# Kernel tuning notes

Measured on AMD Instinct MI355X. Metric: run time of the kernel, lower is better.

The kernel has to match this reference:

```python
import jax, jax.numpy as jnp
import numpy as np

BATCH, SEQ, NUM_SUB, CB_SIZE, SUB_DIM = 8, 2048, 16, 1024, 64
EMB_DIM = NUM_SUB * SUB_DIM  # 1024


def setup_inputs() -> dict:
    key = jax.random.key(0)
    k1, k2 = jax.random.split(key)
    embeddings = jax.random.normal(k1, (BATCH, SEQ, EMB_DIM), dtype=jnp.float32)
    # stacked PQ codebooks: [num_subspaces, codebook_size, subspace_dim]
    codebooks = jax.random.normal(k2, (NUM_SUB, CB_SIZE, SUB_DIM), dtype=jnp.float32)
    return {"embeddings": embeddings, "codebooks": codebooks}


def reference(embeddings, codebooks):
    B, S, D = embeddings.shape
    M, K, d = codebooks.shape
    # [N, M, d] tokens split into subspaces
    x = embeddings.reshape(-1, M, d)
    x2 = jnp.sum(x * x, axis=-1, keepdims=True)            # [N, M, 1]
    c2 = jnp.sum(codebooks * codebooks, axis=-1)           # [M, K]
    xc = jnp.einsum('nmd,mkd->nmk', x, codebooks)          # [N, M, K]
    dist2 = x2 - 2.0 * xc + c2[None, :, :]
    indices = jnp.argmin(dist2, axis=-1)                   # [N, M] (argmin of sqdist == argmin of cdist)
    # gather nearest codeword per subspace: [N, M, d]
    quantized = jnp.take_along_axis(
        codebooks[None, :, :, :],                          # [1, M, K, d]
        indices[:, :, None, None],                         # [N, M, 1, 1]
        axis=2,
    )[:, :, 0, :]
    quantized = quantized.reshape(B, S, D)
    indices = indices.reshape(B, S, M).astype(jnp.int64)
    return quantized, indices
```

## Files before the change

### kernel.cpp

```cpp
#include <hip/hip_runtime.h>
#include <hip/hip_bf16.h>

#pragma clang fp contract(off)

#define NSUB 16
#define CBK  1024
#define SDIM 64
#define EMB  1024
#define NTOK 16384
#define TOKB 128
#define MARGIN 5e-3f

typedef __attribute__((ext_vector_type(8))) short bf16x8;
typedef __attribute__((ext_vector_type(4))) float f32x4;

__device__ __forceinline__ float fmul(float a, float b) { return __fmul_rn(a, b); }
__device__ __forceinline__ float fadd(float a, float b) { return __fadd_rn(a, b); }
__device__ __forceinline__ float fsub(float a, float b) { return __fsub_rn(a, b); }

__device__ __forceinline__ float np_sq64(const float* v) {
    float r[8];
    #pragma unroll
    for (int j = 0; j < 8; ++j) r[j] = fmul(v[j], v[j]);
    #pragma unroll
    for (int b = 1; b < 8; ++b) {
        #pragma unroll
        for (int j = 0; j < 8; ++j)
            r[j] = fadd(r[j], fmul(v[b * 8 + j], v[b * 8 + j]));
    }
    return fadd(fadd(fadd(r[0], r[1]), fadd(r[2], r[3])),
                fadd(fadd(r[4], r[5]), fadd(r[6], r[7])));
}

__device__ __forceinline__ void split_bf16(float v, short& hi, short& lo) {
    __hip_bfloat16 h = __float2bfloat16(v);
    float hf = __bfloat162float(h);
    __hip_bfloat16 e = __float2bfloat16(__fsub_rn(v, hf));
    hi = *(short*)&h;
    lo = *(short*)&e;
}

typedef const __attribute__((address_space(1))) unsigned int gu32;
typedef __attribute__((address_space(3))) unsigned int lu32;
__device__ __forceinline__ void stage16(const void* g, void* l) {
    __builtin_amdgcn_global_load_lds((gu32*)g, (lu32*)l, 16, 0, 0);
}

__global__ __launch_bounds__(256)
void prep_kernel(const float* __restrict__ cb,
                 unsigned short* __restrict__ bpack,
                 float* __restrict__ c2g)
{
    const int bx = blockIdx.x;
    const int m  = blockIdx.y;
    const int t  = threadIdx.x;
    const int w  = t >> 6, l = t & 63;
    const int tc = bx * 2 + (w & 1);
    const int c  = w >> 1;
    const int cw = tc * 16 + (l & 15);
    const int dq = (l >> 4) * 8;

    {
        const float* src = cb + ((size_t)m * CBK + cw) * SDIM + c * 32 + dq;
        bf16x8 hv, lv;
        #pragma unroll
        for (int j = 0; j < 8; ++j) {
            short h, e; split_bf16(-2.0f * src[j], h, e);
            hv[j] = h; lv[j] = e;
        }
        size_t base = (((size_t)(m * 64 + tc) * 2 + c) * 2) * 512 + (size_t)l * 8;
        *(bf16x8*)(bpack + base)       = hv;
        *(bf16x8*)(bpack + base + 512) = lv;
    }
    if (t < 32) {
        const int row = bx * 32 + t;
        c2g[m * CBK + row] = np_sq64(cb + ((size_t)m * CBK + row) * SDIM);
    }
}

__global__ __launch_bounds__(256)
void idx_transpose_kernel(const float* __restrict__ iws,
                          float* __restrict__ iout)
{
    const int tok = blockIdx.x * 256 + threadIdx.x;
    float v[NSUB];
    #pragma unroll
    for (int m = 0; m < NSUB; ++m)
        v[m] = iws[(size_t)m * NTOK + tok];
    float* dst = iout + (size_t)tok * NSUB;
    #pragma unroll
    for (int c = 0; c < 4; ++c)
        *(f32x4*)(dst + c * 4) = *(f32x4*)(v + c * 4);
}

__global__ __launch_bounds__(256, 4)
void pq_mfma_kernel(const float* __restrict__ emb,
                    const float* __restrict__ cb,
                    const unsigned short* __restrict__ bpack,
                    const float* __restrict__ c2g,
                    float* __restrict__ qout,
                    float* __restrict__ iws)
{
    __shared__ __align__(16) unsigned short bs[2][4 * 2048];
    __shared__ float C2s[CBK];
    __shared__ int   bestk_s[TOKB];
    __shared__ int   flag_s[TOKB];
    __shared__ int   cnt_s;

    const int rank = blockIdx.x;
    const int m    = rank & 15;
    const int tok0 = (rank >> 4) * TOKB;

    const int t = threadIdx.x, w = t >> 6, l = t & 63;
    const int ln15 = l & 15, q = l >> 4;

    if (t == 0) cnt_s = 0;
    *(f32x4*)(C2s + t * 4) = *(const f32x4*)(c2g + m * CBK + t * 4);

    const unsigned short* gB = bpack + (size_t)m * 64 * 2048;

    {
        const unsigned short* src = gB + t * 8;
        #pragma unroll
        for (int j = 0; j < 4; ++j)
            stage16(src + j * 2048, &bs[0][j * 2048 + t * 8]);
    }

    bf16x8 xh[2][2], xl[2][2];
    #pragma unroll
    for (int r = 0; r < 2; ++r) {
        const int tok = tok0 + w * 32 + r * 16 + ln15;
        #pragma unroll
        for (int c = 0; c < 2; ++c) {
            const float* src = emb + (size_t)tok * EMB + m * SDIM + c * 32 + q * 8;
            float4 v0 = *(const float4*)(src);
            float4 v1 = *(const float4*)(src + 4);
            float vv[8] = {v0.x,v0.y,v0.z,v0.w,v1.x,v1.y,v1.z,v1.w};
            #pragma unroll
            for (int j = 0; j < 8; ++j) {
                short h, e; split_bf16(vv[j], h, e);
                xh[r][c][j] = h; xl[r][c][j] = e;
            }
        }
    }

    float v1t[2][4], v2t[2][4]; int k1t[2][4];
    #pragma unroll
    for (int r = 0; r < 2; ++r)
        #pragma unroll
        for (int g = 0; g < 4; ++g) { v1t[r][g] = 3.4e38f; v2t[r][g] = 3.4e38f; k1t[r][g] = 0; }

    __syncthreads();

#define COMPUTE_TILE(B0, B1, B2, B3, TC)                                        \
    {                                                                           \
        const int kk = (TC) * 16 + ln15;                                        \
        const float c2v = C2s[kk];                                              \
        _Pragma("unroll")                                                       \
        for (int r = 0; r < 2; ++r) {                                           \
            f32x4 acc = {c2v, c2v, c2v, c2v};                                   \
            acc = __builtin_amdgcn_mfma_f32_16x16x32_bf16(xh[r][0], B0, acc, 0, 0, 0); \
            acc = __builtin_amdgcn_mfma_f32_16x16x32_bf16(xh[r][1], B2, acc, 0, 0, 0); \
            acc = __builtin_amdgcn_mfma_f32_16x16x32_bf16(xl[r][0], B0, acc, 0, 0, 0); \
            acc = __builtin_amdgcn_mfma_f32_16x16x32_bf16(xl[r][1], B2, acc, 0, 0, 0); \
            acc = __builtin_amdgcn_mfma_f32_16x16x32_bf16(xh[r][0], B1, acc, 0, 0, 0); \
            acc = __builtin_amdgcn_mfma_f32_16x16x32_bf16(xh[r][1], B3, acc, 0, 0, 0); \
            _Pragma("unroll")                                                   \
            for (int g = 0; g < 4; ++g) {                                       \
                float s = acc[g];                                               \
                v2t[r][g] = fminf(v2t[r][g], fmaxf(s, v1t[r][g]));              \
                bool lt = s < v1t[r][g];                                        \
                v1t[r][g] = lt ? s : v1t[r][g];                                 \
                k1t[r][g] = lt ? kk : k1t[r][g];                                \
            }                                                                   \
        }                                                                       \
    }

    for (int ph = 0; ph < 16; ++ph) {
        const int buf = ph & 1;
        if (ph < 15) {
            const unsigned short* src = gB + (size_t)(ph + 1) * 8192 + t * 8;
            #pragma unroll
            for (int j = 0; j < 4; ++j)
                stage16(src + j * 2048, &bs[buf ^ 1][j * 2048 + t * 8]);
        }
        #pragma unroll
        for (int j = 0; j < 4; ++j) {
            const int tc = ph * 4 + j;
            const unsigned short* bp = &bs[buf][j * 2048 + l * 8];
            bf16x8 B0 = *(const bf16x8*)(bp);
            bf16x8 B1 = *(const bf16x8*)(bp + 512);
            bf16x8 B2 = *(const bf16x8*)(bp + 1024);
            bf16x8 B3 = *(const bf16x8*)(bp + 1536);
            COMPUTE_TILE(B0, B1, B2, B3, tc)
        }
        __syncthreads();
    }
#undef COMPUTE_TILE

    #pragma unroll
    for (int r = 0; r < 2; ++r) {
        #pragma unroll
        for (int g = 0; g < 4; ++g) {
            float v1 = v1t[r][g], v2 = v2t[r][g]; int k1 = k1t[r][g];
            #pragma unroll
            for (int mask = 1; mask < 16; mask <<= 1) {
                float ov1 = __shfl_xor(v1, mask);
                float ov2 = __shfl_xor(v2, mask);
                int   ok1 = __shfl_xor(k1, mask);
                if (ov1 < v1 || (ov1 == v1 && ok1 < k1)) {
                    v2 = fminf(v1, ov2);
                    v1 = ov1; k1 = ok1;
                } else {
                    v2 = fminf(v2, ov1);
                }
            }
            if (ln15 == 0) {
                const int token = w * 32 + r * 16 + q * 4 + g;
                if (v2 - v1 <= MARGIN) {
                    int slot = atomicAdd(&cnt_s, 1);
                    flag_s[slot] = token;
                } else {
                    bestk_s[token] = k1;
                    iws[(size_t)m * NTOK + tok0 + token] = (float)k1;
                }
            }
        }
    }
    __syncthreads();

    const int nflag = cnt_s;
    for (int g0 = w * 16; g0 < nflag; g0 += 64) {
        const int slotL = g0 + ln15;
        const int tokL  = flag_s[slotL < nflag ? slotL : g0];
        bf16x8 fxh[2], fxl[2];
        #pragma unroll
        for (int c = 0; c < 2; ++c) {
            const float* src = emb + (size_t)(tok0 + tokL) * EMB + m * SDIM + c * 32 + q * 8;
            float4 v0 = *(const float4*)(src);
            float4 v1 = *(const float4*)(src + 4);
            float vv[8] = {v0.x,v0.y,v0.z,v0.w,v1.x,v1.y,v1.z,v1.w};
            #pragma unroll
            for (int j = 0; j < 8; ++j) {
                short h, e; split_bf16(vv[j], h, e);
                fxh[c][j] = h; fxl[c][j] = e;
            }
        }

        unsigned long long cmask[4] = {0ull, 0ull, 0ull, 0ull};
        float v1r[4] = {3.4e38f, 3.4e38f, 3.4e38f, 3.4e38f};
        const unsigned short* bp0 = gB + (size_t)l * 8;
        bf16x8 Bc0 = *(const bf16x8*)(bp0);
        bf16x8 Bc1 = *(const bf16x8*)(bp0 + 512);
        bf16x8 Bc2 = *(const bf16x8*)(bp0 + 1024);
        bf16x8 Bc3 = *(const bf16x8*)(bp0 + 1536);
        #pragma unroll 2
        for (int tc = 0; tc < 64; ++tc) {
            bf16x8 Bn0, Bn1, Bn2, Bn3;
            if (tc < 63) {
                const unsigned short* bpn = gB + (size_t)(tc + 1) * 2048 + (size_t)l * 8;
                Bn0 = *(const bf16x8*)(bpn);
                Bn1 = *(const bf16x8*)(bpn + 512);
                Bn2 = *(const bf16x8*)(bpn + 1024);
                Bn3 = *(const bf16x8*)(bpn + 1536);
            }
            const int kk = tc * 16 + ln15;
            const float c2v = C2s[kk];
            f32x4 acc = {c2v, c2v, c2v, c2v};
            acc = __builtin_amdgcn_mfma_f32_16x16x32_bf16(fxh[0], Bc0, acc, 0, 0, 0);
            acc = __builtin_amdgcn_mfma_f32_16x16x32_bf16(fxh[1], Bc2, acc, 0, 0, 0);
            acc = __builtin_amdgcn_mfma_f32_16x16x32_bf16(fxl[0], Bc0, acc, 0, 0, 0);
            acc = __builtin_amdgcn_mfma_f32_16x16x32_bf16(fxl[1], Bc2, acc, 0, 0, 0);
            acc = __builtin_amdgcn_mfma_f32_16x16x32_bf16(fxh[0], Bc1, acc, 0, 0, 0);
            acc = __builtin_amdgcn_mfma_f32_16x16x32_bf16(fxh[1], Bc3, acc, 0, 0, 0);
            #pragma unroll
            for (int g = 0; g < 4; ++g) {
                float s = acc[g];
                bool cand = (s <= v1r[g] + MARGIN);
                cmask[g] |= cand ? (1ull << tc) : 0ull;
                v1r[g] = fminf(v1r[g], s);
            }
            Bc0 = Bn0; Bc1 = Bn1; Bc2 = Bn2; Bc3 = Bn3;
        }

        #pragma unroll
        for (int g = 0; g < 4; ++g) {
            const int slot = g0 + q * 4 + g;
            if (slot < nflag) {
                const int token = flag_s[slot];
                const float* xrow = emb + (size_t)(tok0 + token) * EMB + m * SDIM;
                unsigned long long msk = cmask[g];
                const float x2v = np_sq64(xrow);
                float bv = 3.4e38f; int bk = CBK;
                while (msk) {
                    const int tc = __builtin_ctzll(msk);
                    msk &= msk - 1;
                    const int k = tc * 16 + ln15;
                    const float* crow = cb + ((size_t)m * CBK + k) * SDIM;
                    float acc = 0.f;
                    #pragma unroll
                    for (int i = 0; i < 16; ++i) {
                        float4 c4 = *(const float4*)(crow + 4 * i);
                        float4 x4 = *(const float4*)(xrow + 4 * i);
                        acc = __fmaf_rn(x4.x, c4.x, acc);
                        acc = __fmaf_rn(x4.y, c4.y, acc);
                        acc = __fmaf_rn(x4.z, c4.z, acc);
                        acc = __fmaf_rn(x4.w, c4.w, acc);
                    }
                    const float dist = fadd(fsub(x2v, fmul(2.f, acc)), C2s[k]);
                    if (dist < bv) { bv = dist; bk = k; }
                }
                #pragma unroll
                for (int mask = 1; mask < 16; mask <<= 1) {
                    float ov = __shfl_xor(bv, mask);
                    int   ok = __shfl_xor(bk, mask);
                    if (ov < bv || (ov == bv && ok < bk)) { bv = ov; bk = ok; }
                }
                if (ln15 == 0) {
                    bestk_s[token] = bk;
                    iws[(size_t)m * NTOK + tok0 + token] = (float)bk;
                }
            }
        }
    }
    __syncthreads();

    {
        const int tok = t >> 1, d0 = (t & 1) * 32;
        const int bk  = bestk_s[tok];
        const float* src = cb + ((size_t)m * CBK + bk) * SDIM + d0;
        float* dst = qout + (size_t)(tok0 + tok) * EMB + m * SDIM + d0;
        #pragma unroll
        for (int i = 0; i < 8; ++i)
            *(float4*)(dst + 4 * i) = *(const float4*)(src + 4 * i);
    }
}

extern "C" void kernel_launch(void* const* d_in, const int* in_sizes, int n_in,
                              void* d_out, int out_size, void* d_ws, size_t ws_size,
                              hipStream_t stream) {
    const float* emb = (const float*)d_in[0];
    const float* cb  = (const float*)d_in[1];
    float* qout = (float*)d_out;
    float* iout = (float*)d_out + (size_t)NTOK * EMB;

    unsigned short* bpack = (unsigned short*)d_ws;
    float* c2g = (float*)((char*)d_ws + 4u * 1024u * 1024u);
    float* iws = (float*)((char*)d_ws + 4u * 1024u * 1024u + 64u * 1024u);

    prep_kernel<<<dim3(32, 16), 256, 0, stream>>>(cb, bpack, c2g);
    pq_mfma_kernel<<<dim3(NTOK / TOKB * NSUB), 256, 0, stream>>>(
        emb, cb, bpack, c2g, qout, iws);
    idx_transpose_kernel<<<dim3(NTOK / 256), 256, 0, stream>>>(iws, iout);
}
```

Baseline: 253.8 us.

## Replace double-buffered codebook staging with six-slot ring pipeline and staggered start

```diff
diff --git a/kernel.cpp b/kernel.cpp
--- a/kernel.cpp
+++ b/kernel.cpp
@@ -101,7 +101,7 @@
                     float* __restrict__ qout,
                     float* __restrict__ iws)
 {
-    __shared__ __align__(16) unsigned short bs[2][4 * 2048];
+    __shared__ __align__(16) unsigned short bs[6][2048];
     __shared__ float C2s[CBK];
     __shared__ int   bestk_s[TOKB];
     __shared__ int   flag_s[TOKB];
@@ -118,13 +118,6 @@
     *(f32x4*)(C2s + t * 4) = *(const f32x4*)(c2g + m * CBK + t * 4);
 
     const unsigned short* gB = bpack + (size_t)m * 64 * 2048;
-
-    {
-        const unsigned short* src = gB + t * 8;
-        #pragma unroll
-        for (int j = 0; j < 4; ++j)
-            stage16(src + j * 2048, &bs[0][j * 2048 + t * 8]);
-    }
 
     bf16x8 xh[2][2], xl[2][2];
     #pragma unroll
@@ -152,51 +145,74 @@
 
     __syncthreads();
 
-#define COMPUTE_TILE(B0, B1, B2, B3, TC)                                        \
+    const int start = (rank * 11) & 63;
+
+#define STAGE_TILE(PT, SLOT)                                                    \
+    stage16(gB + (size_t)(PT) * 2048 + (size_t)t * 8, &bs[(SLOT)][t * 8])
+
+    int pw = start;
+    #pragma unroll
+    for (int j = 0; j < 4; ++j) { STAGE_TILE(pw, j); pw = (pw + 1) & 63; }
+
+#define PQ_STEP(WAITN, DO_STAGE)                                                \
     {                                                                           \
-        const int kk = (TC) * 16 + ln15;                                        \
+        if (DO_STAGE) {                                                         \
+            STAGE_TILE(pw, wslot);                                              \
+            pw = (pw + 1) & 63;                                                 \
+            wslot = (wslot == 5) ? 0 : wslot + 1;                               \
+        }                                                                       \
+        asm volatile("s_waitcnt vmcnt(" #WAITN ")" ::: "memory");               \
+        __builtin_amdgcn_s_barrier();                                           \
+        __builtin_amdgcn_sched_barrier(0);                                      \
+        const unsigned short* bp = &bs[rslot][l * 8];                           \
+        bf16x8 B0 = *(const bf16x8*)(bp);                                       \
+        bf16x8 B1 = *(const bf16x8*)(bp + 512);                                 \
+        bf16x8 B2 = *(const bf16x8*)(bp + 1024);                                \
+        bf16x8 B3 = *(const bf16x8*)(bp + 1536);                                \
+        const int kk = pr * 16 + ln15;                                          \
         const float c2v = C2s[kk];                                              \
+        f32x4 a0 = {c2v, c2v, c2v, c2v};                                        \
+        f32x4 a1 = {c2v, c2v, c2v, c2v};                                        \
+        __builtin_amdgcn_s_setprio(1);                                          \
+        a0 = __builtin_amdgcn_mfma_f32_16x16x32_bf16(xh[0][0], B0, a0, 0, 0, 0);\
+        a1 = __builtin_amdgcn_mfma_f32_16x16x32_bf16(xh[1][0], B0, a1, 0, 0, 0);\
+        a0 = __builtin_amdgcn_mfma_f32_16x16x32_bf16(xh[0][1], B2, a0, 0, 0, 0);\
+        a1 = __builtin_amdgcn_mfma_f32_16x16x32_bf16(xh[1][1], B2, a1, 0, 0, 0);\
+        a0 = __builtin_amdgcn_mfma_f32_16x16x32_bf16(xl[0][0], B0, a0, 0, 0, 0);\
+        a1 = __builtin_amdgcn_mfma_f32_16x16x32_bf16(xl[1][0], B0, a1, 0, 0, 0);\
+        a0 = __builtin_amdgcn_mfma_f32_16x16x32_bf16(xl[0][1], B2, a0, 0, 0, 0);\
+        a1 = __builtin_amdgcn_mfma_f32_16x16x32_bf16(xl[1][1], B2, a1, 0, 0, 0);\
+        a0 = __builtin_amdgcn_mfma_f32_16x16x32_bf16(xh[0][0], B1, a0, 0, 0, 0);\
+        a1 = __builtin_amdgcn_mfma_f32_16x16x32_bf16(xh[1][0], B1, a1, 0, 0, 0);\
+        a0 = __builtin_amdgcn_mfma_f32_16x16x32_bf16(xh[0][1], B3, a0, 0, 0, 0);\
+        a1 = __builtin_amdgcn_mfma_f32_16x16x32_bf16(xh[1][1], B3, a1, 0, 0, 0);\
+        __builtin_amdgcn_s_setprio(0);                                          \
         _Pragma("unroll")                                                       \
-        for (int r = 0; r < 2; ++r) {                                           \
-            f32x4 acc = {c2v, c2v, c2v, c2v};                                   \
-            acc = __builtin_amdgcn_mfma_f32_16x16x32_bf16(xh[r][0], B0, acc, 0, 0, 0); \
-            acc = __builtin_amdgcn_mfma_f32_16x16x32_bf16(xh[r][1], B2, acc, 0, 0, 0); \
-            acc = __builtin_amdgcn_mfma_f32_16x16x32_bf16(xl[r][0], B0, acc, 0, 0, 0); \
-            acc = __builtin_amdgcn_mfma_f32_16x16x32_bf16(xl[r][1], B2, acc, 0, 0, 0); \
-            acc = __builtin_amdgcn_mfma_f32_16x16x32_bf16(xh[r][0], B1, acc, 0, 0, 0); \
-            acc = __builtin_amdgcn_mfma_f32_16x16x32_bf16(xh[r][1], B3, acc, 0, 0, 0); \
-            _Pragma("unroll")                                                   \
-            for (int g = 0; g < 4; ++g) {                                       \
-                float s = acc[g];                                               \
-                v2t[r][g] = fminf(v2t[r][g], fmaxf(s, v1t[r][g]));              \
-                bool lt = s < v1t[r][g];                                        \
-                v1t[r][g] = lt ? s : v1t[r][g];                                 \
-                k1t[r][g] = lt ? kk : k1t[r][g];                                \
-            }                                                                   \
+        for (int g = 0; g < 4; ++g) {                                           \
+            float s0 = a0[g];                                                   \
+            v2t[0][g] = fminf(v2t[0][g], fmaxf(s0, v1t[0][g]));                 \
+            bool lt0 = s0 < v1t[0][g];                                          \
+            v1t[0][g] = lt0 ? s0 : v1t[0][g];                                   \
+            k1t[0][g] = lt0 ? kk : k1t[0][g];                                   \
+            float s1 = a1[g];                                                   \
+            v2t[1][g] = fminf(v2t[1][g], fmaxf(s1, v1t[1][g]));                 \
+            bool lt1 = s1 < v1t[1][g];                                          \
+            v1t[1][g] = lt1 ? s1 : v1t[1][g];                                   \
+            k1t[1][g] = lt1 ? kk : k1t[1][g];                                   \
         }                                                                       \
-    }
-
-    for (int ph = 0; ph < 16; ++ph) {
-        const int buf = ph & 1;
-        if (ph < 15) {
-            const unsigned short* src = gB + (size_t)(ph + 1) * 8192 + t * 8;
-            #pragma unroll
-            for (int j = 0; j < 4; ++j)
-                stage16(src + j * 2048, &bs[buf ^ 1][j * 2048 + t * 8]);
-        }
-        #pragma unroll
-        for (int j = 0; j < 4; ++j) {
-            const int tc = ph * 4 + j;
-            const unsigned short* bp = &bs[buf][j * 2048 + l * 8];
-            bf16x8 B0 = *(const bf16x8*)(bp);
-            bf16x8 B1 = *(const bf16x8*)(bp + 512);
-            bf16x8 B2 = *(const bf16x8*)(bp + 1024);
-            bf16x8 B3 = *(const bf16x8*)(bp + 1536);
-            COMPUTE_TILE(B0, B1, B2, B3, tc)
-        }
-        __syncthreads();
-    }
-#undef COMPUTE_TILE
+        pr = (pr + 1) & 63;                                                     \
+        rslot = (rslot == 5) ? 0 : rslot + 1;                                   \
+    }
+
+    int rslot = 0, wslot = 4, pr = start;
+    for (int s = 0; s < 60; ++s)
+        PQ_STEP(4, true)
+    PQ_STEP(3, false)
+    PQ_STEP(2, false)
+    PQ_STEP(1, false)
+    PQ_STEP(0, false)
+#undef PQ_STEP
+#undef STAGE_TILE
 
     #pragma unroll
     for (int r = 0; r < 2; ++r) {
```

Result: slower. 270.7 us (+6.7%).

## Use single bf16 MFMA screening with per-token adaptive refinement margin

Applied to the files above, without the earlier changes.

```diff
diff --git a/kernel.cpp b/kernel.cpp
--- a/kernel.cpp
+++ b/kernel.cpp
@@ -9,7 +9,8 @@
 #define EMB  1024
 #define NTOK 16384
 #define TOKB 128
-#define MARGIN 5e-3f
+#define MCOEF  0.036f
+#define MFLOOR 0.01f
 
 typedef __attribute__((ext_vector_type(8))) short bf16x8;
 typedef __attribute__((ext_vector_type(4))) float f32x4;
@@ -18,6 +19,11 @@
 __device__ __forceinline__ float fadd(float a, float b) { return __fadd_rn(a, b); }
 __device__ __forceinline__ float fsub(float a, float b) { return __fsub_rn(a, b); }
 
+__device__ __forceinline__ short bf16rn(float v) {
+    __hip_bfloat16 h = __float2bfloat16(v);
+    return *(short*)&h;
+}
+
 __device__ __forceinline__ float np_sq64(const float* v) {
     float r[8];
     #pragma unroll
@@ -30,14 +36,6 @@
     }
     return fadd(fadd(fadd(r[0], r[1]), fadd(r[2], r[3])),
                 fadd(fadd(r[4], r[5]), fadd(r[6], r[7])));
-}
-
-__device__ __forceinline__ void split_bf16(float v, short& hi, short& lo) {
-    __hip_bfloat16 h = __float2bfloat16(v);
-    float hf = __bfloat162float(h);
-    __hip_bfloat16 e = __float2bfloat16(__fsub_rn(v, hf));
-    hi = *(short*)&h;
-    lo = *(short*)&e;
 }
 
 typedef const __attribute__((address_space(1))) unsigned int gu32;
@@ -62,15 +60,12 @@
 
     {
         const float* src = cb + ((size_t)m * CBK + cw) * SDIM + c * 32 + dq;
-        bf16x8 hv, lv;
-        #pragma unroll
-        for (int j = 0; j < 8; ++j) {
-            short h, e; split_bf16(-2.0f * src[j], h, e);
-            hv[j] = h; lv[j] = e;
-        }
-        size_t base = (((size_t)(m * 64 + tc) * 2 + c) * 2) * 512 + (size_t)l * 8;
-        *(bf16x8*)(bpack + base)       = hv;
-        *(bf16x8*)(bpack + base + 512) = lv;
+        bf16x8 hv;
+        #pragma unroll
+        for (int j = 0; j < 8; ++j)
+            hv[j] = bf16rn(-2.0f * src[j]);
+        size_t base = (((size_t)(m * 64 + tc) * 2 + c)) * 512 + (size_t)l * 8;
+        *(bf16x8*)(bpack + base) = hv;
     }
     if (t < 32) {
         const int row = bx * 32 + t;
@@ -101,11 +96,13 @@
                     float* __restrict__ qout,
                     float* __restrict__ iws)
 {
-    __shared__ __align__(16) unsigned short bs[2][4 * 2048];
+    __shared__ __align__(16) unsigned short bs[2][4 * 1024];
     __shared__ float C2s[CBK];
+    __shared__ float x2s[TOKB];
     __shared__ int   bestk_s[TOKB];
     __shared__ int   flag_s[TOKB];
     __shared__ int   cnt_s;
+    __shared__ int   c2maxb;
 
     const int rank = blockIdx.x;
     const int m    = rank & 15;
@@ -114,22 +111,25 @@
     const int t = threadIdx.x, w = t >> 6, l = t & 63;
     const int ln15 = l & 15, q = l >> 4;
 
-    if (t == 0) cnt_s = 0;
-    *(f32x4*)(C2s + t * 4) = *(const f32x4*)(c2g + m * CBK + t * 4);
-
-    const unsigned short* gB = bpack + (size_t)m * 64 * 2048;
+    if (t == 0) { cnt_s = 0; c2maxb = 0; }
+    f32x4 c2quad = *(const f32x4*)(c2g + m * CBK + t * 4);
+    *(f32x4*)(C2s + t * 4) = c2quad;
+    float c2lm = fmaxf(fmaxf(c2quad[0], c2quad[1]), fmaxf(c2quad[2], c2quad[3]));
+
+    const unsigned short* gB = bpack + (size_t)m * 64 * 1024;
 
     {
         const unsigned short* src = gB + t * 8;
         #pragma unroll
-        for (int j = 0; j < 4; ++j)
+        for (int j = 0; j < 2; ++j)
             stage16(src + j * 2048, &bs[0][j * 2048 + t * 8]);
     }
 
-    bf16x8 xh[2][2], xl[2][2];
+    bf16x8 xh[2][2];
     #pragma unroll
     for (int r = 0; r < 2; ++r) {
         const int tok = tok0 + w * 32 + r * 16 + ln15;
+        float x2p = 0.f;
         #pragma unroll
         for (int c = 0; c < 2; ++c) {
             const float* src = emb + (size_t)tok * EMB + m * SDIM + c * 32 + q * 8;
@@ -138,10 +138,13 @@
             float vv[8] = {v0.x,v0.y,v0.z,v0.w,v1.x,v1.y,v1.z,v1.w};
             #pragma unroll
             for (int j = 0; j < 8; ++j) {
-                short h, e; split_bf16(vv[j], h, e);
-                xh[r][c][j] = h; xl[r][c][j] = e;
-            }
-        }
+                xh[r][c][j] = bf16rn(vv[j]);
+                x2p += vv[j] * vv[j];
+            }
+        }
+        x2p += __shfl_xor(x2p, 16);
+        x2p += __shfl_xor(x2p, 32);
+        if (l < 16) x2s[w * 32 + r * 16 + l] = x2p;
     }
 
     float v1t[2][4], v2t[2][4]; int k1t[2][4];
@@ -151,52 +154,48 @@
         for (int g = 0; g < 4; ++g) { v1t[r][g] = 3.4e38f; v2t[r][g] = 3.4e38f; k1t[r][g] = 0; }
 
     __syncthreads();
-
-#define COMPUTE_TILE(B0, B1, B2, B3, TC)                                        \
-    {                                                                           \
-        const int kk = (TC) * 16 + ln15;                                        \
-        const float c2v = C2s[kk];                                              \
-        _Pragma("unroll")                                                       \
-        for (int r = 0; r < 2; ++r) {                                           \
-            f32x4 acc = {c2v, c2v, c2v, c2v};                                   \
-            acc = __builtin_amdgcn_mfma_f32_16x16x32_bf16(xh[r][0], B0, acc, 0, 0, 0); \
-            acc = __builtin_amdgcn_mfma_f32_16x16x32_bf16(xh[r][1], B2, acc, 0, 0, 0); \
-            acc = __builtin_amdgcn_mfma_f32_16x16x32_bf16(xl[r][0], B0, acc, 0, 0, 0); \
-            acc = __builtin_amdgcn_mfma_f32_16x16x32_bf16(xl[r][1], B2, acc, 0, 0, 0); \
-            acc = __builtin_amdgcn_mfma_f32_16x16x32_bf16(xh[r][0], B1, acc, 0, 0, 0); \
-            acc = __builtin_amdgcn_mfma_f32_16x16x32_bf16(xh[r][1], B3, acc, 0, 0, 0); \
-            _Pragma("unroll")                                                   \
-            for (int g = 0; g < 4; ++g) {                                       \
-                float s = acc[g];                                               \
-                v2t[r][g] = fminf(v2t[r][g], fmaxf(s, v1t[r][g]));              \
-                bool lt = s < v1t[r][g];                                        \
-                v1t[r][g] = lt ? s : v1t[r][g];                                 \
-                k1t[r][g] = lt ? kk : k1t[r][g];                                \
-            }                                                                   \
-        }                                                                       \
-    }
+    atomicMax(&c2maxb, __float_as_int(c2lm));
 
     for (int ph = 0; ph < 16; ++ph) {
         const int buf = ph & 1;
         if (ph < 15) {
-            const unsigned short* src = gB + (size_t)(ph + 1) * 8192 + t * 8;
-            #pragma unroll
-            for (int j = 0; j < 4; ++j)
+            const unsigned short* src = gB + (size_t)(ph + 1) * 4096 + t * 8;
+            #pragma unroll
+            for (int j = 0; j < 2; ++j)
                 stage16(src + j * 2048, &bs[buf ^ 1][j * 2048 + t * 8]);
         }
         #pragma unroll
         for (int j = 0; j < 4; ++j) {
             const int tc = ph * 4 + j;
-            const unsigned short* bp = &bs[buf][j * 2048 + l * 8];
+            const unsigned short* bp = &bs[buf][j * 1024 + l * 8];
             bf16x8 B0 = *(const bf16x8*)(bp);
             bf16x8 B1 = *(const bf16x8*)(bp + 512);
-            bf16x8 B2 = *(const bf16x8*)(bp + 1024);
-            bf16x8 B3 = *(const bf16x8*)(bp + 1536);
-            COMPUTE_TILE(B0, B1, B2, B3, tc)
+            const int kk = tc * 16 + ln15;
+            const float c2v = C2s[kk];
+            f32x4 a0 = {c2v, c2v, c2v, c2v};
+            f32x4 a1 = {c2v, c2v, c2v, c2v};
+            a0 = __builtin_amdgcn_mfma_f32_16x16x32_bf16(xh[0][0], B0, a0, 0, 0, 0);
+            a1 = __builtin_amdgcn_mfma_f32_16x16x32_bf16(xh[1][0], B0, a1, 0, 0, 0);
+            a0 = __builtin_amdgcn_mfma_f32_16x16x32_bf16(xh[0][1], B1, a0, 0, 0, 0);
+            a1 = __builtin_amdgcn_mfma_f32_16x16x32_bf16(xh[1][1], B1, a1, 0, 0, 0);
+            #pragma unroll
+            for (int g = 0; g < 4; ++g) {
+                float s0 = a0[g];
+                v2t[0][g] = fminf(v2t[0][g], fmaxf(s0, v1t[0][g]));
+                bool lt0 = s0 < v1t[0][g];
+                v1t[0][g] = lt0 ? s0 : v1t[0][g];
+                k1t[0][g] = lt0 ? kk : k1t[0][g];
+                float s1 = a1[g];
+                v2t[1][g] = fminf(v2t[1][g], fmaxf(s1, v1t[1][g]));
+                bool lt1 = s1 < v1t[1][g];
+                v1t[1][g] = lt1 ? s1 : v1t[1][g];
+                k1t[1][g] = lt1 ? kk : k1t[1][g];
+            }
         }
         __syncthreads();
     }
-#undef COMPUTE_TILE
+
+    const float c2mx = __int_as_float(c2maxb);
 
     #pragma unroll
     for (int r = 0; r < 2; ++r) {
@@ -217,7 +216,8 @@
             }
             if (ln15 == 0) {
                 const int token = w * 32 + r * 16 + q * 4 + g;
-                if (v2 - v1 <= MARGIN) {
+                const float Mtok = MCOEF * sqrtf(x2s[token] * c2mx) + MFLOOR;
+                if (v2 - v1 <= Mtok) {
                     int slot = atomicAdd(&cnt_s, 1);
                     flag_s[slot] = token;
                 } else {
@@ -233,7 +233,7 @@
     for (int g0 = w * 16; g0 < nflag; g0 += 64) {
         const int slotL = g0 + ln15;
         const int tokL  = flag_s[slotL < nflag ? slotL : g0];
-        bf16x8 fxh[2], fxl[2];
+        bf16x8 fxh[2];
         #pragma unroll
         for (int c = 0; c < 2; ++c) {
             const float* src = emb + (size_t)(tok0 + tokL) * EMB + m * SDIM + c * 32 + q * 8;
@@ -241,10 +241,16 @@
             float4 v1 = *(const float4*)(src + 4);
             float vv[8] = {v0.x,v0.y,v0.z,v0.w,v1.x,v1.y,v1.z,v1.w};
             #pragma unroll
-            for (int j = 0; j < 8; ++j) {
-                short h, e; split_bf16(vv[j], h, e);
-                fxh[c][j] = h; fxl[c][j] = e;
-            }
+            for (int j = 0; j < 8; ++j)
+                fxh[c][j] = bf16rn(vv[j]);
+        }
+
+        float Mg[4];
+        #pragma unroll
+        for (int g = 0; g < 4; ++g) {
+            const int slot = g0 + q * 4 + g;
+            const int tokg = flag_s[slot < nflag ? slot : g0];
+            Mg[g] = MCOEF * sqrtf(x2s[tokg] * c2mx) + MFLOOR;
         }
 
         unsigned long long cmask[4] = {0ull, 0ull, 0ull, 0ull};
@@ -252,35 +258,27 @@
         const unsigned short* bp0 = gB + (size_t)l * 8;
         bf16x8 Bc0 = *(const bf16x8*)(bp0);
         bf16x8 Bc1 = *(const bf16x8*)(bp0 + 512);
-        bf16x8 Bc2 = *(const bf16x8*)(bp0 + 1024);
-        bf16x8 Bc3 = *(const bf16x8*)(bp0 + 1536);
         #pragma unroll 2
         for (int tc = 0; tc < 64; ++tc) {
-            bf16x8 Bn0, Bn1, Bn2, Bn3;
+            bf16x8 Bn0, Bn1;
             if (tc < 63) {
-                const unsigned short* bpn = gB + (size_t)(tc + 1) * 2048 + (size_t)l * 8;
+                const unsigned short* bpn = gB + (size_t)(tc + 1) * 1024 + (size_t)l * 8;
                 Bn0 = *(const bf16x8*)(bpn);
                 Bn1 = *(const bf16x8*)(bpn + 512);
-                Bn2 = *(const bf16x8*)(bpn + 1024);
-                Bn3 = *(const bf16x8*)(bpn + 1536);
             }
             const int kk = tc * 16 + ln15;
             const float c2v = C2s[kk];
             f32x4 acc = {c2v, c2v, c2v, c2v};
             acc = __builtin_amdgcn_mfma_f32_16x16x32_bf16(fxh[0], Bc0, acc, 0, 0, 0);
-            acc = __builtin_amdgcn_mfma_f32_16x16x32_bf16(fxh[1], Bc2, acc, 0, 0, 0);
-            acc = __builtin_amdgcn_mfma_f32_16x16x32_bf16(fxl[0], Bc0, acc, 0, 0, 0);
-            acc = __builtin_amdgcn_mfma_f32_16x16x32_bf16(fxl[1], Bc2, acc, 0, 0, 0);
-            acc = __builtin_amdgcn_mfma_f32_16x16x32_bf16(fxh[0], Bc1, acc, 0, 0, 0);
-            acc = __builtin_amdgcn_mfma_f32_16x16x32_bf16(fxh[1], Bc3, acc, 0, 0, 0);
+            acc = __builtin_amdgcn_mfma_f32_16x16x32_bf16(fxh[1], Bc1, acc, 0, 0, 0);
             #pragma unroll
             for (int g = 0; g < 4; ++g) {
                 float s = acc[g];
-                bool cand = (s <= v1r[g] + MARGIN);
+                bool cand = (s <= v1r[g] + Mg[g]);
                 cmask[g] |= cand ? (1ull << tc) : 0ull;
                 v1r[g] = fminf(v1r[g], s);
             }
-            Bc0 = Bn0; Bc1 = Bn1; Bc2 = Bn2; Bc3 = Bn3;
+            Bc0 = Bn0; Bc1 = Bn1;
         }
 
         #pragma unroll
@@ -345,8 +343,8 @@
     float* iout = (float*)d_out + (size_t)NTOK * EMB;
 
     unsigned short* bpack = (unsigned short*)d_ws;
-    float* c2g = (float*)((char*)d_ws + 4u * 1024u * 1024u);
-    float* iws = (float*)((char*)d_ws + 4u * 1024u * 1024u + 64u * 1024u);
+    float* c2g = (float*)((char*)d_ws + 2u * 1024u * 1024u);
+    float* iws = (float*)((char*)d_ws + 2u * 1024u * 1024u + 64u * 1024u);
 
     prep_kernel<<<dim3(32, 16), 256, 0, stream>>>(cb, bpack, c2g);
     pq_mfma_kernel<<<dim3(NTOK / TOKB * NSUB), 256, 0, stream>>>(
```

Result: slower. 706.8 us (+178.5%).
